# Kernel tuning notes

Hardware: AMD Instinct MI355X
Metric: run time of the kernel (lower is better)

The kernel has to match this reference:

```python
import jax, jax.numpy as jnp
import numpy as np

N_NODES = 50000
N_EDGES = 1000000
C = 32          # nchannels (multiplicity of each irrep)
NBESSEL = 8
WEIGHT_NUMEL = 3 * C  # three uvu paths: 0e->0e, 0e->1o, 0e->2e


def setup_inputs() -> dict:
    key = jax.random.key(0)
    ks = jax.random.split(key, 12)
    inp = {
        "lenght": jax.random.uniform(ks[0], (N_EDGES, NBESSEL), dtype=jnp.float32),
        "node_features": jax.random.normal(ks[1], (N_NODES, C), dtype=jnp.float32),
        "edge_attributes": jax.random.normal(ks[2], (N_EDGES, 9), dtype=jnp.float32),
        "edge_index": jax.random.randint(ks[3], (2, N_EDGES), 0, N_NODES, dtype=jnp.int64),
        # FullyConnectedNet([8, 6, 6, 6, 96]) weights (e3nn stores unnormalized W, divides by sqrt(fan_in))
        "fcn_w0": jax.random.normal(ks[4], (NBESSEL, 6), dtype=jnp.float32),
        "fcn_w1": jax.random.normal(ks[5], (6, 6), dtype=jnp.float32),
        "fcn_w2": jax.random.normal(ks[6], (6, 6), dtype=jnp.float32),
        "fcn_w3": jax.random.normal(ks[7], (6, WEIGHT_NUMEL), dtype=jnp.float32),
        # equivariant Linear irreps_mid -> irreps_out: one [C, C] mixing matrix per l in {0,1,2}
        "lin_w0": jax.random.normal(ks[8], (C, C), dtype=jnp.float32),
        "lin_w1": jax.random.normal(ks[9], (C, C), dtype=jnp.float32),
        "lin_w2": jax.random.normal(ks[10], (C, C), dtype=jnp.float32),
    }
    return inp


def _fcn(x, w0, w1, w2, w3):
    # e3nn FullyConnectedNet: normalized linear layers with SiLU on hidden layers
    for w in (w0, w1, w2):
        x = jax.nn.silu((x @ w) * (1.0 / np.float32(np.sqrt(w.shape[0]))))
    return (x @ w3) * (1.0 / np.float32(np.sqrt(w3.shape[0])))


def reference(lenght, node_features, edge_attributes, edge_index,
              fcn_w0, fcn_w1, fcn_w2, fcn_w3, lin_w0, lin_w1, lin_w2):
    sender = edge_index[0]
    receiver = edge_index[1]
    num_nodes = node_features.shape[0]
    c = node_features.shape[1]
    e = lenght.shape[0]

    # per-edge tensor-product weights: [E, 3C]
    tp_w = _fcn(lenght, fcn_w0, fcn_w1, fcn_w2, fcn_w3)
    w0, w1, w2 = tp_w[:, :c], tp_w[:, c:2 * c], tp_w[:, 2 * c:]

    x = node_features[sender]                       # gather: [E, C]
    y0 = edge_attributes[:, 0:1]                    # 0e: [E, 1]
    y1 = edge_attributes[:, 1:4]                    # 1o: [E, 3]
    y2 = edge_attributes[:, 4:9]                    # 2e: [E, 5]

    # uvu tensor product, CG for 0e x l -> l is identity
    m0 = w0 * x * y0                                # [E, C]
    m1 = (w1 * x)[:, :, None] * y1[:, None, :]      # [E, C, 3]
    m2 = (w2 * x)[:, :, None] * y2[:, None, :]      # [E, C, 5]
    mij = jnp.concatenate(
        [m0, m1.reshape(e, 3 * c), m2.reshape(e, 5 * c)], axis=1)  # [E, 9C]

    # scatter_sum over receivers
    msg = jax.ops.segment_sum(mij, receiver, num_segments=num_nodes)  # [N, 9C]

    # equivariant Linear (per-l channel mixing, 1/sqrt(fan_in) normalization)
    inv = 1.0 / np.float32(np.sqrt(c))
    o0 = (msg[:, :c] @ lin_w0) * inv                                   # [N, C]
    o1 = jnp.einsum('nci,cd->ndi', msg[:, c:4 * c].reshape(num_nodes, c, 3), lin_w1) * inv
    o2 = jnp.einsum('nci,cd->ndi', msg[:, 4 * c:].reshape(num_nodes, c, 5), lin_w2) * inv
    return jnp.concatenate(
        [o0, o1.reshape(num_nodes, 3 * c), o2.reshape(num_nodes, 5 * c)], axis=1)
```

## Files before the change

kernel.cpp:

```cpp
#include <hip/hip_runtime.h>
#include <math.h>

#define N_NODES 50000
#define N_EDGES 1000000
#define CCH     32
#define ROW     288
#define SCAN_BLOCKS 196

__global__ __launch_bounds__(256) void hist_kernel(
    const int* __restrict__ edge_index, int* __restrict__ deg)
{
    const int e = blockIdx.x * 256 + threadIdx.x;
    if (e >= N_EDGES) return;
    atomicAdd(&deg[edge_index[N_EDGES + e]], 1);
}

__global__ __launch_bounds__(256) void scan_local_kernel(
    const int* __restrict__ deg, int* __restrict__ lexcl, int* __restrict__ blocksum)
{
    __shared__ int s[256];
    const int t = threadIdx.x;
    const int gid = blockIdx.x * 256 + t;
    const int v = (gid < N_NODES) ? deg[gid] : 0;
    s[t] = v;
    __syncthreads();
    for (int ofs = 1; ofs < 256; ofs <<= 1) {
        int w = (t >= ofs) ? s[t - ofs] : 0;
        __syncthreads();
        s[t] += w;
        __syncthreads();
    }
    if (gid < N_NODES) lexcl[gid] = s[t] - v;
    if (t == 255) blocksum[blockIdx.x] = s[255];
}

__global__ __launch_bounds__(256) void scan_top_kernel(
    const int* __restrict__ blocksum, int* __restrict__ blockpref)
{
    __shared__ int s[256];
    const int t = threadIdx.x;
    const int v = (t < SCAN_BLOCKS) ? blocksum[t] : 0;
    s[t] = v;
    __syncthreads();
    for (int ofs = 1; ofs < 256; ofs <<= 1) {
        int w = (t >= ofs) ? s[t - ofs] : 0;
        __syncthreads();
        s[t] += w;
        __syncthreads();
    }
    if (t < SCAN_BLOCKS) blockpref[t] = s[t] - v;
}

__global__ __launch_bounds__(256) void scan_addback_kernel(
    const int* __restrict__ lexcl, const int* __restrict__ blockpref,
    int* __restrict__ offset, int* __restrict__ cursor)
{
    const int gid = blockIdx.x * 256 + threadIdx.x;
    if (gid >= N_NODES) return;
    const int base = blockpref[blockIdx.x] + lexcl[gid];
    offset[gid] = base;
    cursor[gid] = base;
}

__global__ __launch_bounds__(256) void pack_kernel(
    const float* __restrict__ lenght,
    const float* __restrict__ edge_attr,
    const int*   __restrict__ edge_index,
    const float* __restrict__ fw0,
    const float* __restrict__ fw1,
    const float* __restrict__ fw2,
    int*         __restrict__ cursor,
    float4*      __restrict__ rec)
{
    __shared__ float s_w[120];
    for (int i = threadIdx.x; i < 120; i += 256)
        s_w[i] = (i < 48) ? fw0[i] : (i < 84) ? fw1[i - 48] : fw2[i - 84];
    __syncthreads();
    const float* sw0 = s_w;
    const float* sw1 = s_w + 48;
    const float* sw2 = s_w + 84;

    const int e = blockIdx.x * 256 + threadIdx.x;
    if (e >= N_EDGES) return;

    const float inv8 = 0.35355339059327373f;
    const float inv6 = 0.4082482904638631f;

    float len[8];
    const float4 l0 = ((const float4*)(lenght + (long long)e * 8))[0];
    const float4 l1 = ((const float4*)(lenght + (long long)e * 8))[1];
    len[0]=l0.x; len[1]=l0.y; len[2]=l0.z; len[3]=l0.w;
    len[4]=l1.x; len[5]=l1.y; len[6]=l1.z; len[7]=l1.w;

    float h0[6], h1[6], h2[6];
    #pragma unroll
    for (int j = 0; j < 6; ++j) {
        float a = 0.f;
        #pragma unroll
        for (int k = 0; k < 8; ++k) a += len[k] * sw0[k * 6 + j];
        a *= inv8;
        h0[j] = a / (1.f + __expf(-a));
    }
    #pragma unroll
    for (int j = 0; j < 6; ++j) {
        float a = 0.f;
        #pragma unroll
        for (int k = 0; k < 6; ++k) a += h0[k] * sw1[k * 6 + j];
        a *= inv6;
        h1[j] = a / (1.f + __expf(-a));
    }
    #pragma unroll
    for (int j = 0; j < 6; ++j) {
        float a = 0.f;
        #pragma unroll
        for (int k = 0; k < 6; ++k) a += h1[k] * sw2[k * 6 + j];
        a *= inv6;
        h2[j] = a * inv6 / (1.f + __expf(-a));
    }

    const float* ea = edge_attr + (long long)e * 9;
    float y[9];
    #pragma unroll
    for (int i = 0; i < 9; ++i) y[i] = ea[i];

    const int snd = edge_index[e];
    const int r   = edge_index[N_EDGES + e];
    const int p   = atomicAdd(&cursor[r], 1);

    float4* rp = rec + (long long)p * 4;
    rp[0] = make_float4(h2[0], h2[1], h2[2], h2[3]);
    rp[1] = make_float4(h2[4], h2[5], y[0], y[1]);
    rp[2] = make_float4(y[2], y[3], y[4], y[5]);
    rp[3] = make_float4(y[6], y[7], y[8], __int_as_float(snd));
}

__global__ __launch_bounds__(256) void gather_kernel(
    const float4* __restrict__ rec,
    const float*  __restrict__ node_features,
    const int*    __restrict__ offset,
    const int*    __restrict__ deg,
    const float*  __restrict__ fw3,
    const float*  __restrict__ lw0,
    const float*  __restrict__ lw1,
    const float*  __restrict__ lw2,
    float*        __restrict__ out)
{
    __shared__ float s_lw0[1024], s_lw1[1024], s_lw2[1024];
    for (int i = threadIdx.x; i < 1024; i += 256) {
        s_lw0[i] = lw0[i];
        s_lw1[i] = lw1[i];
        s_lw2[i] = lw2[i];
    }
    __syncthreads();

    const int wave = threadIdx.x >> 6;
    const int l    = threadIdx.x & 63;
    const int c    = l & 31;
    const int h    = l >> 5;
    const int node = blockIdx.x * 4 + wave;

    float f3a[6], f3b[6], f3c[6];
    #pragma unroll
    for (int k = 0; k < 6; ++k) {
        f3a[k] = fw3[k * 96 + c];
        f3b[k] = fw3[k * 96 + 32 + c];
        f3c[k] = fw3[k * 96 + 64 + c];
    }

    const int off = offset[node];
    const int dg  = deg[node];

    float acc[9] = {0.f,0.f,0.f,0.f,0.f,0.f,0.f,0.f,0.f};

    int j = h;
    float4 r0, r1, r2, r3;
    float  xq = 0.f;
    if (j < dg) {
        const float4* rp = rec + (long long)(off + j) * 4;
        r0 = rp[0]; r1 = rp[1]; r2 = rp[2]; r3 = rp[3];
        xq = node_features[(long long)__float_as_int(r3.w) * CCH + c];
    }
    while (j < dg) {
        const int jn = j + 2;
        float4 n0, n1, n2, n3;
        if (jn < dg) {
            const float4* rp = rec + (long long)(off + jn) * 4;
            n0 = rp[0]; n1 = rp[1]; n2 = rp[2]; n3 = rp[3];
        }

        const float w0c = r0.x*f3a[0] + r0.y*f3a[1] + r0.z*f3a[2]
                        + r0.w*f3a[3] + r1.x*f3a[4] + r1.y*f3a[5];
        const float w1c = r0.x*f3b[0] + r0.y*f3b[1] + r0.z*f3b[2]
                        + r0.w*f3b[3] + r1.x*f3b[4] + r1.y*f3b[5];
        const float w2c = r0.x*f3c[0] + r0.y*f3c[1] + r0.z*f3c[2]
                        + r0.w*f3c[3] + r1.x*f3c[4] + r1.y*f3c[5];

        const float x = xq;
        acc[0] += (w0c * x) * r1.z;
        const float a1 = w1c * x;
        acc[1] += a1 * r1.w;
        acc[2] += a1 * r2.x;
        acc[3] += a1 * r2.y;
        const float a2 = w2c * x;
        acc[4] += a2 * r2.z;
        acc[5] += a2 * r2.w;
        acc[6] += a2 * r3.x;
        acc[7] += a2 * r3.y;
        acc[8] += a2 * r3.z;

        if (jn < dg)
            xq = node_features[(long long)__float_as_int(n3.w) * CCH + c];
        r0 = n0; r1 = n1; r2 = n2; r3 = n3;
        j = jn;
    }

    #pragma unroll
    for (int k = 0; k < 9; ++k) acc[k] += __shfl_down(acc[k], 32);

    const int d = c;
    float o0 = 0.f;
    float o1[3] = {0.f, 0.f, 0.f};
    float o2[5] = {0.f, 0.f, 0.f, 0.f, 0.f};
    for (int cc = h * 16; cc < h * 16 + 16; ++cc) {
        const float m0 = __shfl(acc[0], cc);
        const float m1 = __shfl(acc[1], cc);
        const float m2 = __shfl(acc[2], cc);
        const float m3 = __shfl(acc[3], cc);
        const float m4 = __shfl(acc[4], cc);
        const float m5 = __shfl(acc[5], cc);
        const float m6 = __shfl(acc[6], cc);
        const float m7 = __shfl(acc[7], cc);
        const float m8 = __shfl(acc[8], cc);
        o0 += m0 * s_lw0[cc * 32 + d];
        const float w1 = s_lw1[cc * 32 + d];
        o1[0] += m1 * w1; o1[1] += m2 * w1; o1[2] += m3 * w1;
        const float w2 = s_lw2[cc * 32 + d];
        o2[0] += m4 * w2; o2[1] += m5 * w2; o2[2] += m6 * w2;
        o2[3] += m7 * w2; o2[4] += m8 * w2;
    }

    o0 += __shfl_down(o0, 32);
    #pragma unroll
    for (int i = 0; i < 3; ++i) o1[i] += __shfl_down(o1[i], 32);
    #pragma unroll
    for (int i = 0; i < 5; ++i) o2[i] += __shfl_down(o2[i], 32);

    if (h == 0) {
        const float inv32 = 0.17677669529663687f;
        float* op = out + (long long)node * ROW;
        op[d] = o0 * inv32;
        #pragma unroll
        for (int i = 0; i < 3; ++i) op[32 + d * 3 + i] = o1[i] * inv32;
        #pragma unroll
        for (int i = 0; i < 5; ++i) op[128 + d * 5 + i] = o2[i] * inv32;
    }
}

extern "C" void kernel_launch(void* const* d_in, const int* in_sizes, int n_in,
                              void* d_out, int out_size, void* d_ws, size_t ws_size,
                              hipStream_t stream)
{
    const float* lenght = (const float*)d_in[0];
    const float* nf     = (const float*)d_in[1];
    const float* ea     = (const float*)d_in[2];
    const int*   ei     = (const int*)d_in[3];
    const float* fw0    = (const float*)d_in[4];
    const float* fw1    = (const float*)d_in[5];
    const float* fw2    = (const float*)d_in[6];
    const float* fw3    = (const float*)d_in[7];
    const float* lw0    = (const float*)d_in[8];
    const float* lw1    = (const float*)d_in[9];
    const float* lw2    = (const float*)d_in[10];
    float* out = (float*)d_out;

    char* ws = (char*)d_ws;
    float4* rec    = (float4*)ws; ws += (size_t)N_EDGES * 4 * sizeof(float4);
    int* deg       = (int*)ws;    ws += (size_t)N_NODES * sizeof(int);
    int* offset    = (int*)ws;    ws += (size_t)N_NODES * sizeof(int);
    int* cursor    = (int*)ws;    ws += (size_t)N_NODES * sizeof(int);
    int* lexcl     = (int*)ws;    ws += (size_t)N_NODES * sizeof(int);
    int* blocksum  = (int*)ws;    ws += (size_t)SCAN_BLOCKS * sizeof(int);
    int* blockpref = (int*)ws;    ws += (size_t)SCAN_BLOCKS * sizeof(int);

    hipMemsetAsync(deg, 0, (size_t)N_NODES * sizeof(int), stream);

    const int EB = (N_EDGES + 255) / 256;
    hist_kernel        <<<EB, 256, 0, stream>>>(ei, deg);
    scan_local_kernel  <<<SCAN_BLOCKS, 256, 0, stream>>>(deg, lexcl, blocksum);
    scan_top_kernel    <<<1, 256, 0, stream>>>(blocksum, blockpref);
    scan_addback_kernel<<<SCAN_BLOCKS, 256, 0, stream>>>(lexcl, blockpref, offset, cursor);
    pack_kernel        <<<EB, 256, 0, stream>>>(lenght, ea, ei, fw0, fw1, fw2, cursor, rec);
    gather_kernel      <<<N_NODES / 4, 256, 0, stream>>>(
        rec, nf, offset, deg, fw3, lw0, lw1, lw2, out);
}
```

Baseline: 381.8 us.

## Fuse three-pass scan into one kernel and process four nodes per wave in gather

Replaces the local/top/addback scan kernels with one scan kernel in which each block reduces all preceding degrees itself to get its base offset. This drops two launches and the intermediate arrays. The gather kernel now gives each wave four consecutive nodes, reads five offsets with one vector load, and prefetches the next node's first record. This amortizes the fw3 register loads and per-wave setup at the cost of fewer waves in flight. The redundant prefix reduction grows with block index, adding O(N·blocks) reads.

```diff
diff --git a/kernel.cpp b/kernel.cpp
--- a/kernel.cpp
+++ b/kernel.cpp
@@ -15,12 +15,29 @@
     atomicAdd(&deg[edge_index[N_EDGES + e]], 1);
 }
 
-__global__ __launch_bounds__(256) void scan_local_kernel(
-    const int* __restrict__ deg, int* __restrict__ lexcl, int* __restrict__ blocksum)
+__global__ __launch_bounds__(256) void scan_kernel(
+    const int* __restrict__ deg, int* __restrict__ offset, int* __restrict__ cursor)
 {
     __shared__ int s[256];
+    __shared__ int s_base;
     const int t = threadIdx.x;
-    const int gid = blockIdx.x * 256 + t;
+    const int b = blockIdx.x;
+
+    int part = 0;
+    for (int i = t; i < b * 256; i += 256) part += deg[i];
+    s[t] = part;
+    __syncthreads();
+    #pragma unroll
+    for (int ofs = 128; ofs > 0; ofs >>= 1) {
+        if (t < ofs) s[t] += s[t + ofs];
+        __syncthreads();
+    }
+    if (t == 0) s_base = s[0];
+    __syncthreads();
+    const int base = s_base;
+    __syncthreads();
+
+    const int gid = b * 256 + t;
     const int v = (gid < N_NODES) ? deg[gid] : 0;
     s[t] = v;
     __syncthreads();
@@ -30,36 +47,12 @@
         s[t] += w;
         __syncthreads();
     }
-    if (gid < N_NODES) lexcl[gid] = s[t] - v;
-    if (t == 255) blocksum[blockIdx.x] = s[255];
-}
-
-__global__ __launch_bounds__(256) void scan_top_kernel(
-    const int* __restrict__ blocksum, int* __restrict__ blockpref)
-{
-    __shared__ int s[256];
-    const int t = threadIdx.x;
-    const int v = (t < SCAN_BLOCKS) ? blocksum[t] : 0;
-    s[t] = v;
-    __syncthreads();
-    for (int ofs = 1; ofs < 256; ofs <<= 1) {
-        int w = (t >= ofs) ? s[t - ofs] : 0;
-        __syncthreads();
-        s[t] += w;
-        __syncthreads();
-    }
-    if (t < SCAN_BLOCKS) blockpref[t] = s[t] - v;
-}
-
-__global__ __launch_bounds__(256) void scan_addback_kernel(
-    const int* __restrict__ lexcl, const int* __restrict__ blockpref,
-    int* __restrict__ offset, int* __restrict__ cursor)
-{
-    const int gid = blockIdx.x * 256 + threadIdx.x;
-    if (gid >= N_NODES) return;
-    const int base = blockpref[blockIdx.x] + lexcl[gid];
-    offset[gid] = base;
-    cursor[gid] = base;
+    const int excl = s[t] - v;
+    if (gid < N_NODES) {
+        offset[gid] = base + excl;
+        cursor[gid] = base + excl;
+    }
+    if (b == SCAN_BLOCKS - 1 && t == 255) offset[N_NODES] = base + s[255];
 }
 
 __global__ __launch_bounds__(256) void pack_kernel(
@@ -138,7 +131,6 @@
     const float4* __restrict__ rec,
     const float*  __restrict__ node_features,
     const int*    __restrict__ offset,
-    const int*    __restrict__ deg,
     const float*  __restrict__ fw3,
     const float*  __restrict__ lw0,
     const float*  __restrict__ lw1,
@@ -157,7 +149,8 @@
     const int l    = threadIdx.x & 63;
     const int c    = l & 31;
     const int h    = l >> 5;
-    const int node = blockIdx.x * 4 + wave;
+    const int wid  = blockIdx.x * 4 + wave;
+    const int base = wid * 4;
 
     float f3a[6], f3b[6], f3c[6];
     #pragma unroll
@@ -167,92 +160,112 @@
         f3c[k] = fw3[k * 96 + 64 + c];
     }
 
-    const int off = offset[node];
-    const int dg  = deg[node];
-
-    float acc[9] = {0.f,0.f,0.f,0.f,0.f,0.f,0.f,0.f,0.f};
-
-    int j = h;
+    int offs[5];
+    {
+        const int4 o4 = *(const int4*)(offset + base);
+        offs[0] = o4.x; offs[1] = o4.y; offs[2] = o4.z; offs[3] = o4.w;
+        offs[4] = offset[base + 4];
+    }
+
     float4 r0, r1, r2, r3;
-    float  xq = 0.f;
-    if (j < dg) {
-        const float4* rp = rec + (long long)(off + j) * 4;
+    if (h < offs[1] - offs[0]) {
+        const float4* rp = rec + (long long)(offs[0] + h) * 4;
         r0 = rp[0]; r1 = rp[1]; r2 = rp[2]; r3 = rp[3];
-        xq = node_features[(long long)__float_as_int(r3.w) * CCH + c];
-    }
-    while (j < dg) {
-        const int jn = j + 2;
-        float4 n0, n1, n2, n3;
-        if (jn < dg) {
-            const float4* rp = rec + (long long)(off + jn) * 4;
-            n0 = rp[0]; n1 = rp[1]; n2 = rp[2]; n3 = rp[3];
+    }
+
+    const float inv32 = 0.17677669529663687f;
+    const int d = c;
+
+    #pragma unroll 1
+    for (int k = 0; k < 4; ++k) {
+        const int off = offs[k];
+        const int dg  = offs[k + 1] - off;
+
+        float acc[9] = {0.f,0.f,0.f,0.f,0.f,0.f,0.f,0.f,0.f};
+        float xq = 0.f;
+        if (h < dg)
+            xq = node_features[(long long)__float_as_int(r3.w) * CCH + c];
+
+        int j = h;
+        while (j < dg) {
+            const int jn = j + 2;
+            float4 n0, n1, n2, n3;
+            if (jn < dg) {
+                const float4* rp = rec + (long long)(off + jn) * 4;
+                n0 = rp[0]; n1 = rp[1]; n2 = rp[2]; n3 = rp[3];
+            }
+
+            const float w0c = r0.x*f3a[0] + r0.y*f3a[1] + r0.z*f3a[2]
+                            + r0.w*f3a[3] + r1.x*f3a[4] + r1.y*f3a[5];
+            const float w1c = r0.x*f3b[0] + r0.y*f3b[1] + r0.z*f3b[2]
+                            + r0.w*f3b[3] + r1.x*f3b[4] + r1.y*f3b[5];
+            const float w2c = r0.x*f3c[0] + r0.y*f3c[1] + r0.z*f3c[2]
+                            + r0.w*f3c[3] + r1.x*f3c[4] + r1.y*f3c[5];
+
+            const float x = xq;
+            acc[0] += (w0c * x) * r1.z;
+            const float a1 = w1c * x;
+            acc[1] += a1 * r1.w;
+            acc[2] += a1 * r2.x;
+            acc[3] += a1 * r2.y;
+            const float a2 = w2c * x;
+            acc[4] += a2 * r2.z;
+            acc[5] += a2 * r2.w;
+            acc[6] += a2 * r3.x;
+            acc[7] += a2 * r3.y;
+            acc[8] += a2 * r3.z;
+
+            if (jn < dg)
+                xq = node_features[(long long)__float_as_int(n3.w) * CCH + c];
+            r0 = n0; r1 = n1; r2 = n2; r3 = n3;
+            j = jn;
         }
 
-        const float w0c = r0.x*f3a[0] + r0.y*f3a[1] + r0.z*f3a[2]
-                        + r0.w*f3a[3] + r1.x*f3a[4] + r1.y*f3a[5];
-        const float w1c = r0.x*f3b[0] + r0.y*f3b[1] + r0.z*f3b[2]
-                        + r0.w*f3b[3] + r1.x*f3b[4] + r1.y*f3b[5];
-        const float w2c = r0.x*f3c[0] + r0.y*f3c[1] + r0.z*f3c[2]
-                        + r0.w*f3c[3] + r1.x*f3c[4] + r1.y*f3c[5];
-
-        const float x = xq;
-        acc[0] += (w0c * x) * r1.z;
-        const float a1 = w1c * x;
-        acc[1] += a1 * r1.w;
-        acc[2] += a1 * r2.x;
-        acc[3] += a1 * r2.y;
-        const float a2 = w2c * x;
-        acc[4] += a2 * r2.z;
-        acc[5] += a2 * r2.w;
-        acc[6] += a2 * r3.x;
-        acc[7] += a2 * r3.y;
-        acc[8] += a2 * r3.z;
-
-        if (jn < dg)
-            xq = node_features[(long long)__float_as_int(n3.w) * CCH + c];
-        r0 = n0; r1 = n1; r2 = n2; r3 = n3;
-        j = jn;
-    }
-
-    #pragma unroll
-    for (int k = 0; k < 9; ++k) acc[k] += __shfl_down(acc[k], 32);
-
-    const int d = c;
-    float o0 = 0.f;
-    float o1[3] = {0.f, 0.f, 0.f};
-    float o2[5] = {0.f, 0.f, 0.f, 0.f, 0.f};
-    for (int cc = h * 16; cc < h * 16 + 16; ++cc) {
-        const float m0 = __shfl(acc[0], cc);
-        const float m1 = __shfl(acc[1], cc);
-        const float m2 = __shfl(acc[2], cc);
-        const float m3 = __shfl(acc[3], cc);
-        const float m4 = __shfl(acc[4], cc);
-        const float m5 = __shfl(acc[5], cc);
-        const float m6 = __shfl(acc[6], cc);
-        const float m7 = __shfl(acc[7], cc);
-        const float m8 = __shfl(acc[8], cc);
-        o0 += m0 * s_lw0[cc * 32 + d];
-        const float w1 = s_lw1[cc * 32 + d];
-        o1[0] += m1 * w1; o1[1] += m2 * w1; o1[2] += m3 * w1;
-        const float w2 = s_lw2[cc * 32 + d];
-        o2[0] += m4 * w2; o2[1] += m5 * w2; o2[2] += m6 * w2;
-        o2[3] += m7 * w2; o2[4] += m8 * w2;
-    }
-
-    o0 += __shfl_down(o0, 32);
-    #pragma unroll
-    for (int i = 0; i < 3; ++i) o1[i] += __shfl_down(o1[i], 32);
-    #pragma unroll
-    for (int i = 0; i < 5; ++i) o2[i] += __shfl_down(o2[i], 32);
-
-    if (h == 0) {
-        const float inv32 = 0.17677669529663687f;
-        float* op = out + (long long)node * ROW;
-        op[d] = o0 * inv32;
-        #pragma unroll
-        for (int i = 0; i < 3; ++i) op[32 + d * 3 + i] = o1[i] * inv32;
-        #pragma unroll
-        for (int i = 0; i < 5; ++i) op[128 + d * 5 + i] = o2[i] * inv32;
+        if (k < 3) {
+            if (h < offs[k + 2] - offs[k + 1]) {
+                const float4* rp = rec + (long long)(offs[k + 1] + h) * 4;
+                r0 = rp[0]; r1 = rp[1]; r2 = rp[2]; r3 = rp[3];
+            }
+        }
+
+        #pragma unroll
+        for (int q = 0; q < 9; ++q) acc[q] += __shfl_down(acc[q], 32);
+
+        float o0 = 0.f;
+        float o1[3] = {0.f, 0.f, 0.f};
+        float o2[5] = {0.f, 0.f, 0.f, 0.f, 0.f};
+        for (int cc = h * 16; cc < h * 16 + 16; ++cc) {
+            const float m0 = __shfl(acc[0], cc);
+            const float m1 = __shfl(acc[1], cc);
+            const float m2 = __shfl(acc[2], cc);
+            const float m3 = __shfl(acc[3], cc);
+            const float m4 = __shfl(acc[4], cc);
+            const float m5 = __shfl(acc[5], cc);
+            const float m6 = __shfl(acc[6], cc);
+            const float m7 = __shfl(acc[7], cc);
+            const float m8 = __shfl(acc[8], cc);
+            o0 += m0 * s_lw0[cc * 32 + d];
+            const float w1 = s_lw1[cc * 32 + d];
+            o1[0] += m1 * w1; o1[1] += m2 * w1; o1[2] += m3 * w1;
+            const float w2 = s_lw2[cc * 32 + d];
+            o2[0] += m4 * w2; o2[1] += m5 * w2; o2[2] += m6 * w2;
+            o2[3] += m7 * w2; o2[4] += m8 * w2;
+        }
+
+        o0 += __shfl_down(o0, 32);
+        #pragma unroll
+        for (int i = 0; i < 3; ++i) o1[i] += __shfl_down(o1[i], 32);
+        #pragma unroll
+        for (int i = 0; i < 5; ++i) o2[i] += __shfl_down(o2[i], 32);
+
+        if (h == 0) {
+            float* op = out + (long long)(base + k) * ROW;
+            op[d] = o0 * inv32;
+            #pragma unroll
+            for (int i = 0; i < 3; ++i) op[32 + d * 3 + i] = o1[i] * inv32;
+            #pragma unroll
+            for (int i = 0; i < 5; ++i) op[128 + d * 5 + i] = o2[i] * inv32;
+        }
     }
 }
 
@@ -274,22 +287,17 @@
     float* out = (float*)d_out;
 
     char* ws = (char*)d_ws;
-    float4* rec    = (float4*)ws; ws += (size_t)N_EDGES * 4 * sizeof(float4);
-    int* deg       = (int*)ws;    ws += (size_t)N_NODES * sizeof(int);
-    int* offset    = (int*)ws;    ws += (size_t)N_NODES * sizeof(int);
-    int* cursor    = (int*)ws;    ws += (size_t)N_NODES * sizeof(int);
-    int* lexcl     = (int*)ws;    ws += (size_t)N_NODES * sizeof(int);
-    int* blocksum  = (int*)ws;    ws += (size_t)SCAN_BLOCKS * sizeof(int);
-    int* blockpref = (int*)ws;    ws += (size_t)SCAN_BLOCKS * sizeof(int);
+    float4* rec = (float4*)ws; ws += (size_t)N_EDGES * 4 * sizeof(float4);
+    int* deg    = (int*)ws;    ws += (size_t)N_NODES * sizeof(int);
+    int* offset = (int*)ws;    ws += (size_t)(N_NODES + 4) * sizeof(int);
+    int* cursor = (int*)ws;    ws += (size_t)N_NODES * sizeof(int);
 
     hipMemsetAsync(deg, 0, (size_t)N_NODES * sizeof(int), stream);
 
     const int EB = (N_EDGES + 255) / 256;
-    hist_kernel        <<<EB, 256, 0, stream>>>(ei, deg);
-    scan_local_kernel  <<<SCAN_BLOCKS, 256, 0, stream>>>(deg, lexcl, blocksum);
-    scan_top_kernel    <<<1, 256, 0, stream>>>(blocksum, blockpref);
-    scan_addback_kernel<<<SCAN_BLOCKS, 256, 0, stream>>>(lexcl, blockpref, offset, cursor);
-    pack_kernel        <<<EB, 256, 0, stream>>>(lenght, ea, ei, fw0, fw1, fw2, cursor, rec);
-    gather_kernel      <<<N_NODES / 4, 256, 0, stream>>>(
-        rec, nf, offset, deg, fw3, lw0, lw1, lw2, out);
-}
+    hist_kernel  <<<EB, 256, 0, stream>>>(ei, deg);
+    scan_kernel  <<<SCAN_BLOCKS, 256, 0, stream>>>(deg, offset, cursor);
+    pack_kernel  <<<EB, 256, 0, stream>>>(lenght, ea, ei, fw0, fw1, fw2, cursor, rec);
+    gather_kernel<<<N_NODES / 16, 256, 0, stream>>>(
+        rec, nf, offset, fw3, lw0, lw1, lw2, out);
+}
```

Result: slower. 507.0 us (+32.8%).
